# Kernel optimization log

Hardware: AMD Instinct MI355X
Metric: run time of the kernel (lower is better)

The kernel has to match this reference:

```python
import jax, jax.numpy as jnp
import numpy as np

B, L, D = 2, 1024, 1024
N = 64                 # ssm_state_dim
R = (D + 15) // 16     # dt_rank = ceil(dim/16) = 64
EPS = 1e-6


def setup_inputs() -> dict:
    key = jax.random.key(0)
    ks = jax.random.split(key, 12)
    s = 0.02
    return {
        "x": jax.random.normal(ks[0], (B, L, D), dtype=jnp.float32),
        "norm_w": jnp.ones((D,), jnp.float32),
        "Wx": jax.random.normal(ks[1], (R + 2 * N, D), jnp.float32) * s,
        "dtW": jax.random.normal(ks[2], (D, R), jnp.float32) * s,
        "dtb": jax.random.normal(ks[3], (D,), jnp.float32) * s,
        "A_log": jnp.zeros((D, N), jnp.float32),
        "Dskip": jnp.ones((D,), jnp.float32),
        "Wout": jax.random.normal(ks[4], (D, D), jnp.float32) * s,
        "selW": jax.random.normal(ks[5], (D, D), jnp.float32) * s,
        "selb": jax.random.normal(ks[6], (D,), jnp.float32) * s,
        "sel_gate": jnp.ones((D,), jnp.float32),
        "impW": jax.random.normal(ks[7], (N, D), jnp.float32) * s,
        "impb": jax.random.normal(ks[8], (N,), jnp.float32) * s,
        "gateW": jax.random.normal(ks[9], (D, D), jnp.float32) * s,
        "gateb": jax.random.normal(ks[10], (D,), jnp.float32) * s,
    }


def _rmsnorm(x, w):
    return x * jax.lax.rsqrt(jnp.mean(x * x, axis=-1, keepdims=True) + EPS) * w


def reference(x, norm_w, Wx, dtW, dtb, A_log, Dskip, Wout, selW, selb,
              sel_gate, impW, impb, gateW, gateb):
    xn = _rmsnorm(x, norm_w)                       # [B,L,D]
    xp = jnp.einsum('bld,kd->blk', xn, Wx)         # [B,L,R+2N]
    delta_r = xp[..., :R]
    B_ssm = xp[..., R:R + N]
    C_ssm = xp[..., R + N:]

    # selective masking
    sel = jax.nn.sigmoid((jnp.einsum('bld,kd->blk', xn, selW) + selb) * sel_gate)
    xn = xn * sel
    imp = jax.nn.sigmoid(jnp.einsum('bld,nd->bln', xn, impW) + impb)  # [B,L,N]

    delta = jax.nn.softplus(jnp.einsum('blr,dr->bld', delta_r, dtW) + dtb)  # [B,L,D]
    A = -jnp.exp(A_log)                            # [D,N]

    # gated update
    gate = jax.nn.sigmoid(jnp.einsum('bld,kd->blk', xn, gateW) + gateb)
    xn = xn * gate

    B_ssm = B_ssm * imp
    C_ssm = C_ssm * imp

    def step(h, inp):
        dt, bt, ct, xt = inp                       # [B,D],[B,N],[B,N],[B,D]
        dA = jnp.exp(dt[:, :, None] * A)           # [B,D,N]
        h = dA * h + dt[:, :, None] * bt[:, None, :] * xt[:, :, None]
        y = jnp.einsum('bdn,bn->bd', h, ct)
        return h, y

    h0 = jnp.zeros((B, D, N), x.dtype)
    xs = (jnp.moveaxis(delta, 1, 0), jnp.moveaxis(B_ssm, 1, 0),
          jnp.moveaxis(C_ssm, 1, 0), jnp.moveaxis(xn, 1, 0))
    _, ys = jax.lax.scan(step, h0, xs)             # ys: [L,B,D]
    y = jnp.moveaxis(ys, 0, 1)                     # [B,L,D]

    return jnp.einsum('bld,kd->blk', y + x * Dskip, Wout)
```

## Files before the change

kernel.cpp:

```cpp
#include <hip/hip_runtime.h>

typedef __attribute__((ext_vector_type(8))) short short8;
typedef __attribute__((ext_vector_type(4))) float f32x4;
typedef unsigned short u16;

__device__ __forceinline__ u16 f2bf(float f){
  unsigned int u = __float_as_uint(f);
  u += 0x7FFFu + ((u>>16)&1u);
  return (u16)(u>>16);
}
__device__ __forceinline__ float bf2f(u16 h){
  return __uint_as_float(((unsigned int)h)<<16);
}
__device__ __forceinline__ float sigm(float x){ return 1.f/(1.f+__expf(-x)); }

__device__ __forceinline__ float fexp2(float x){
#if __has_builtin(__builtin_amdgcn_exp2f)
  return __builtin_amdgcn_exp2f(x);
#else
  float r; asm("v_exp_f32 %0, %1" : "=v"(r) : "v"(x)); return r;
#endif
}

__device__ __forceinline__ void gl_lds(const u16* g, u16* l){
  __builtin_amdgcn_global_load_lds(
      (const __attribute__((address_space(1))) void*)g,
      (__attribute__((address_space(3))) void*)l, 16, 0, 0);
}

#define MDIM 2048
#define DDIM 1024
#define KDIM 1024
#define LOG2E 1.44269504f
#define NCHUNK 32
#define TCH 32
#define CVT_TOTAL 3473408

__global__ __launch_bounds__(256) void pre_k(
    const float* __restrict__ x, const float* __restrict__ nw,
    const float* __restrict__ selW, const float* __restrict__ Wx,
    const float* __restrict__ gateW, const float* __restrict__ impW,
    const float* __restrict__ Wout, const float* __restrict__ dtW,
    u16* __restrict__ xn,
    u16* __restrict__ dA, u16* __restrict__ dB, u16* __restrict__ dC,
    u16* __restrict__ dD)
{
  const int bx = blockIdx.x, tid = threadIdx.x;
  if (bx < 2048){
    float4 xv = ((const float4*)(x + (size_t)bx*DDIM))[tid];
    float s = xv.x*xv.x + xv.y*xv.y + xv.z*xv.z + xv.w*xv.w;
    #pragma unroll
    for (int m=1; m<64; m<<=1) s += __shfl_xor(s, m);
    __shared__ float red[4];
    if ((tid&63)==0) red[tid>>6] = s;
    __syncthreads();
    float tot = red[0]+red[1]+red[2]+red[3];
    float rs = rsqrtf(tot*(1.f/1024.f) + 1e-6f);
    float4 wv = ((const float4*)nw)[tid];
    ushort4 o;
    o.x=f2bf(xv.x*rs*wv.x); o.y=f2bf(xv.y*rs*wv.y);
    o.z=f2bf(xv.z*rs*wv.z); o.w=f2bf(xv.w*rs*wv.w);
    ((ushort4*)(xn + (size_t)bx*DDIM))[tid] = o;
  } else {
    int e = ((bx-2048)*256 + tid)*4;
    if (e >= CVT_TOTAL) return;
    const float4* s; u16* d;
    if (e < 1048576){ s=(const float4*)(selW+e); d=dA+e; }
    else if (e < 1245184){ int o=e-1048576; s=(const float4*)(Wx+o); d=dA+1048576+o; }
    else if (e < 2293760){ int o=e-1245184; s=(const float4*)(gateW+o); d=dB+o; }
    else if (e < 2359296){ int o=e-2293760; s=(const float4*)(impW+o); d=dB+1048576+o; }
    else if (e < 3407872){ int o=e-2359296; s=(const float4*)(Wout+o); d=dC+o; }
    else { int o=e-3407872; s=(const float4*)(dtW+o); d=dD+o; }
    float4 v = *s;
    ushort4 ov; ov.x=f2bf(v.x); ov.y=f2bf(v.y); ov.z=f2bf(v.z); ov.w=f2bf(v.w);
    *(ushort4*)d = ov;
  }
}

template<int MODE>
__device__ __forceinline__ void gemm_body(
    u16* smem,
    const u16* __restrict__ X, const u16* __restrict__ W,
    const float* __restrict__ b1, const float* __restrict__ b2,
    const float* __restrict__ b3, const u16* __restrict__ aux,
    u16* __restrict__ oBF, u16* __restrict__ oBF2,
    float* __restrict__ oF1, float* __restrict__ oF2, float* __restrict__ oF3)
{
  u16* const AsP[3] = { smem, smem + 4096, smem + 8192 };
  u16* const BsP[3] = { smem + 12288, smem + 16384, smem + 20480 };
  const int tid = threadIdx.x;
  const int wid = tid>>6, lane = tid&63;
  const int wr = wid>>1, wc = wid&1;
  const int lr = lane&15, lg = lane>>4;

  const int nx = gridDim.x;
  const int nwg = nx*gridDim.y;
  const int lin = blockIdx.y*nx + blockIdx.x;
  const int lt = (lin&7)*(nwg>>3) + (lin>>3);
  const int bm = (lt/nx)*64, bn = (lt%nx)*64;

  f32x4 acc[2][2];
  #pragma unroll
  for (int a0=0;a0<2;++a0)
    #pragma unroll
    for (int b0=0;b0<2;++b0) acc[a0][b0] = (f32x4){0.f,0.f,0.f,0.f};

  const int srow = wid*8 + (lane>>3);
  const int kslot = 8*((lane&7) ^ (lane>>3));
  const u16* ag = X + (size_t)(bm + srow)*KDIM + kslot;
  const u16* bg = W + (size_t)(bn + srow)*KDIM + kslot;
  const int lofs = wid*512;

  auto stage = [&](int buf, int kt){
    gl_lds(ag + kt, AsP[buf] + lofs);
    gl_lds(ag + (size_t)32*KDIM + kt, AsP[buf] + 2048 + lofs);
    gl_lds(bg + kt, BsP[buf] + lofs);
    gl_lds(bg + (size_t)32*KDIM + kt, BsP[buf] + 2048 + lofs);
  };

  stage(0, 0);
  stage(1, 64);
  stage(2, 128);
  asm volatile("s_waitcnt vmcnt(8)" ::: "memory");
  __builtin_amdgcn_s_barrier();

  #pragma unroll
  for (int t=0; t<16; ++t){
    const int cur = t % 3;
    short8 af[2][2], bfr[2][2];
    #pragma unroll
    for (int a0=0;a0<2;++a0){
      const int R = wr*32 + a0*16 + lr;
      #pragma unroll
      for (int kh=0;kh<2;++kh)
        af[a0][kh] = *(const short8*)(AsP[cur] + R*64 + ((kh*32 + lg*8) ^ ((lr&7)<<3)));
    }
    #pragma unroll
    for (int b0=0;b0<2;++b0){
      const int R = wc*32 + b0*16 + lr;
      #pragma unroll
      for (int kh=0;kh<2;++kh)
        bfr[b0][kh] = *(const short8*)(BsP[cur] + R*64 + ((kh*32 + lg*8) ^ ((lr&7)<<3)));
    }
    asm volatile("s_waitcnt lgkmcnt(0)" ::: "memory");
    __builtin_amdgcn_sched_barrier(0);
    __builtin_amdgcn_s_barrier();
    if (t < 13)
      stage(cur, (t+3)*64);
    #pragma unroll
    for (int kh=0;kh<2;++kh)
      #pragma unroll
      for (int a0=0;a0<2;++a0)
        #pragma unroll
        for (int b0=0;b0<2;++b0)
          acc[a0][b0] = __builtin_amdgcn_mfma_f32_16x16x32_bf16(af[a0][kh], bfr[b0][kh], acc[a0][b0], 0, 0, 0);
    __builtin_amdgcn_sched_barrier(0);
    if (t < 13){
      asm volatile("s_waitcnt vmcnt(8)" ::: "memory");
      __builtin_amdgcn_s_barrier();
    } else if (t == 13){
      asm volatile("s_waitcnt vmcnt(4)" ::: "memory");
      __builtin_amdgcn_s_barrier();
    } else if (t == 14){
      asm volatile("s_waitcnt vmcnt(0)" ::: "memory");
      __builtin_amdgcn_s_barrier();
    }
  }

  const int colb = bn + wc*32;
  #pragma unroll
  for (int a0=0;a0<2;++a0){
    const int m0 = bm + wr*32 + a0*16 + lg*4;
    #pragma unroll
    for (int b0=0;b0<2;++b0){
      const int n = colb + b0*16 + lr;
      #pragma unroll
      for (int i=0;i<4;++i){
        const int m = m0 + i;
        float v = acc[a0][b0][i];
        if constexpr (MODE==0){
          if (n < 1024){
            float s = sigm((v + b1[n])*b2[n]);
            float xnv = bf2f(aux[(size_t)m*1024 + n]);
            oBF[(size_t)m*1024 + n] = f2bf(xnv*s);
          } else if (n < 1088){
            oBF2[(size_t)m*64 + (n-1024)] = f2bf(v);
          } else {
            oF2[(size_t)m*128 + (n-1088)] = v;
          }
        } else if constexpr (MODE==1){
          if (n < 1024){
            float g = sigm(v + b1[n]);
            oBF[(size_t)m*1024 + n] = f2bf(bf2f(aux[(size_t)m*1024 + n])*g);
          } else {
            int c = n-1024;
            float it = sigm(v + b2[c]);
            float bb = b3[(size_t)m*128 + c];
            float cc = b3[(size_t)m*128 + 64 + c];
            oF2[(size_t)m*64 + c] = bb*it;
            oF3[(size_t)m*64 + c] = cc*it;
          }
        } else {
          oF1[(size_t)m*1024 + n] = v;
        }
      }
    }
  }
}

template<int MODE>
__global__ __launch_bounds__(256) void gemm_bt(
    const u16* __restrict__ X, const u16* __restrict__ W,
    const float* __restrict__ b1, const float* __restrict__ b2,
    const float* __restrict__ b3, const u16* __restrict__ aux,
    u16* __restrict__ oBF, u16* __restrict__ oBF2,
    float* __restrict__ oF1, float* __restrict__ oF2, float* __restrict__ oF3)
{
  __shared__ __align__(16) u16 pool[24576];
  gemm_body<MODE>(pool, X, W, b1, b2, b3, aux, oBF, oBF2, oF1, oF2, oF3);
}

__global__ __launch_bounds__(256) void gemm1d_k(
    const u16* __restrict__ xn2, const u16* __restrict__ wsB,
    const float* __restrict__ gateb, const float* __restrict__ impb,
    const float* __restrict__ BCb,
    u16* __restrict__ xn316, float* __restrict__ BIp, float* __restrict__ CIp,
    const u16* __restrict__ dr, const u16* __restrict__ dtWb,
    const float* __restrict__ dtb, u16* __restrict__ delta16)
{
  __shared__ __align__(16) u16 pool[24576];
  if (blockIdx.z == 0){
    gemm_body<1>(pool, xn2, wsB, gateb, impb, BCb, xn2,
                 xn316, nullptr, nullptr, BIp, CIp);
    return;
  }
  if (blockIdx.x >= 16) return;
  u16* As = pool;
  u16* Bs = pool + 4096;
  const int tid = threadIdx.x;
  const int wid = tid>>6, lane = tid&63;
  const int wr = wid>>1, wc = wid&1;
  const int lr = lane&15, lg = lane>>4;
  const int bm = blockIdx.y*64, bn = blockIdx.x*64;

  const int srow = wid*8 + (lane>>3);
  const int kslot = 8*((lane&7) ^ (lane>>3));
  const u16* ag = dr   + (size_t)(bm + srow)*64 + kslot;
  const u16* bg = dtWb + (size_t)(bn + srow)*64 + kslot;
  const int lofs = wid*512;

  gl_lds(ag, As + lofs);
  gl_lds(ag + 32*64, As + 2048 + lofs);
  gl_lds(bg, Bs + lofs);
  gl_lds(bg + 32*64, Bs + 2048 + lofs);
  asm volatile("s_waitcnt vmcnt(0)" ::: "memory");
  __builtin_amdgcn_s_barrier();

  f32x4 acc[2][2];
  #pragma unroll
  for (int a0=0;a0<2;++a0)
    #pragma unroll
    for (int b0=0;b0<2;++b0) acc[a0][b0] = (f32x4){0.f,0.f,0.f,0.f};

  short8 af[2][2], bfr[2][2];
  #pragma unroll
  for (int a0=0;a0<2;++a0){
    const int R = wr*32 + a0*16 + lr;
    #pragma unroll
    for (int kh=0;kh<2;++kh)
      af[a0][kh] = *(const short8*)(As + R*64 + ((kh*32 + lg*8) ^ ((lr&7)<<3)));
  }
  #pragma unroll
  for (int b0=0;b0<2;++b0){
    const int R = wc*32 + b0*16 + lr;
    #pragma unroll
    for (int kh=0;kh<2;++kh)
      bfr[b0][kh] = *(const short8*)(Bs + R*64 + ((kh*32 + lg*8) ^ ((lr&7)<<3)));
  }
  #pragma unroll
  for (int kh=0;kh<2;++kh)
    #pragma unroll
    for (int a0=0;a0<2;++a0)
      #pragma unroll
      for (int b0=0;b0<2;++b0)
        acc[a0][b0] = __builtin_amdgcn_mfma_f32_16x16x32_bf16(af[a0][kh], bfr[b0][kh], acc[a0][b0], 0, 0, 0);

  #pragma unroll
  for (int a0=0;a0<2;++a0){
    const int m0 = bm + wr*32 + a0*16 + lg*4;
    #pragma unroll
    for (int b0=0;b0<2;++b0){
      const int n = bn + wc*32 + b0*16 + lr;
      const float bias = dtb[n];
      #pragma unroll
      for (int i=0;i<4;++i){
        float t = acc[a0][b0][i] + bias;
        float sp = fmaxf(t,0.f) + log1pf(__expf(-fabsf(t)));
        delta16[(size_t)(m0+i)*1024 + n] = f2bf(sp);
      }
    }
  }
}

__global__ __launch_bounds__(256) void scan_p1(
    const u16* __restrict__ delta, const u16* __restrict__ xn3,
    const float* __restrict__ BI, const float* __restrict__ A_log,
    u16* __restrict__ hst, float* __restrict__ sumdt)
{
  const int tid = threadIdx.x;
  const int lane = tid & 63;
  const int wv = __builtin_amdgcn_readfirstlane(tid >> 6);
  const int dg = blockIdx.x, c = blockIdx.y, b = blockIdx.z;
  const int d = dg*64 + lane;
  const int nb = wv*16;
  float A2[16], h[16];
  #pragma unroll
  for (int n0=0;n0<4;++n0){
    float4 al = *(const float4*)(A_log + (size_t)d*64 + nb + n0*4);
    A2[n0*4+0] = -__expf(al.x)*LOG2E;
    A2[n0*4+1] = -__expf(al.y)*LOG2E;
    A2[n0*4+2] = -__expf(al.z)*LOG2E;
    A2[n0*4+3] = -__expf(al.w)*LOG2E;
  }
  #pragma unroll
  for (int n=0;n<16;++n) h[n]=0.f;
  const int row0 = b*1024 + c*TCH;
  float sdt = 0.f;
  #pragma unroll 2
  for (int t=0;t<TCH;++t){
    const size_t row = row0 + t;
    float dt = bf2f(delta[row*1024 + d]);
    float xt = bf2f(xn3[row*1024 + d]);
    sdt += dt;
    float k = dt*xt;
    const float* bi = BI + row*64 + nb;
    #pragma unroll
    for (int n=0;n<16;++n)
      h[n] = fexp2(dt*A2[n])*h[n] + k*bi[n];
  }
  if (wv==0) sumdt[(size_t)(c*2+b)*1024 + d] = sdt;
  #pragma unroll
  for (int n=0;n<16;++n)
    hst[(size_t)((c*2+b)*64 + nb + n)*1024 + d] = f2bf(h[n]);
}

__global__ __launch_bounds__(256) void scan_p2(
    const float* __restrict__ A_log, const float* __restrict__ sumdt,
    u16* __restrict__ hst)
{
  int gid = blockIdx.x*256 + threadIdx.x;
  int d = gid & 1023, n = (gid>>10)&63, b = gid>>16;
  float A2 = -__expf(A_log[(size_t)d*64 + n])*LOG2E;
  const size_t hbase = (size_t)b*65536 + n*1024 + d;
  const size_t sbase = (size_t)b*1024 + d;
  float P[NCHUNK], he[NCHUNK];
  #pragma unroll
  for (int c=0;c<NCHUNK;++c){
    P[c]  = fexp2(A2 * sumdt[sbase + (size_t)c*2048]);
    he[c] = bf2f(hst[hbase + (size_t)c*131072]);
  }
  float carry = 0.f;
  #pragma unroll
  for (int c=0;c<NCHUNK;++c){
    hst[hbase + (size_t)c*131072] = f2bf(carry);
    carry = fmaf(P[c], carry, he[c]);
  }
}

__global__ __launch_bounds__(256) void scan_p3(
    const u16* __restrict__ delta, const u16* __restrict__ xn3,
    const float* __restrict__ BI, const float* __restrict__ CI,
    const float* __restrict__ A_log, const float* __restrict__ x,
    const float* __restrict__ Dskip, const u16* __restrict__ hst,
    u16* __restrict__ z)
{
  __shared__ float ypart[4][TCH][64];
  const int tid = threadIdx.x;
  const int lane = tid & 63;
  const int wv = __builtin_amdgcn_readfirstlane(tid >> 6);
  const int dg = blockIdx.x, c = blockIdx.y, b = blockIdx.z;
  const int d = dg*64 + lane;
  const int nb = wv*16;
  float A2[16], h[16];
  #pragma unroll
  for (int n0=0;n0<4;++n0){
    float4 al = *(const float4*)(A_log + (size_t)d*64 + nb + n0*4);
    A2[n0*4+0] = -__expf(al.x)*LOG2E;
    A2[n0*4+1] = -__expf(al.y)*LOG2E;
    A2[n0*4+2] = -__expf(al.z)*LOG2E;
    A2[n0*4+3] = -__expf(al.w)*LOG2E;
  }
  #pragma unroll
  for (int n=0;n<16;++n)
    h[n] = bf2f(hst[(size_t)((c*2+b)*64 + nb + n)*1024 + d]);
  const int row0 = b*1024 + c*TCH;
  #pragma unroll 2
  for (int t=0;t<TCH;++t){
    const size_t row = row0 + t;
    float dt = bf2f(delta[row*1024 + d]);
    float xt = bf2f(xn3[row*1024 + d]);
    float k = dt*xt;
    const float* bi = BI + row*64 + nb;
    const float* ci = CI + row*64 + nb;
    float y0=0.f, y1=0.f, y2=0.f, y3=0.f;
    #pragma unroll
    for (int n=0;n<16;n+=4){
      h[n+0] = fexp2(dt*A2[n+0])*h[n+0] + k*bi[n+0];  y0 += h[n+0]*ci[n+0];
      h[n+1] = fexp2(dt*A2[n+1])*h[n+1] + k*bi[n+1];  y1 += h[n+1]*ci[n+1];
      h[n+2] = fexp2(dt*A2[n+2])*h[n+2] + k*bi[n+2];  y2 += h[n+2]*ci[n+2];
      h[n+3] = fexp2(dt*A2[n+3])*h[n+3] + k*bi[n+3];  y3 += h[n+3]*ci[n+3];
    }
    ypart[wv][t][lane] = (y0+y1)+(y2+y3);
  }
  __syncthreads();
  const int dbase = dg*64;
  #pragma unroll
  for (int i=0;i<8;++i){
    int idx = tid + i*256;
    int t = idx>>6, dl = idx&63;
    size_t row = row0 + t;
    float y = ypart[0][t][dl] + ypart[1][t][dl] + ypart[2][t][dl] + ypart[3][t][dl];
    float xr = x[row*1024 + dbase + dl];
    z[row*1024 + dbase + dl] = f2bf(y + xr*Dskip[dbase+dl]);
  }
}

extern "C" void kernel_launch(void* const* d_in, const int* in_sizes, int n_in,
                              void* d_out, int out_size, void* d_ws, size_t ws_size,
                              hipStream_t stream) {
  const float* x       = (const float*)d_in[0];
  const float* norm_w  = (const float*)d_in[1];
  const float* Wx      = (const float*)d_in[2];
  const float* dtW     = (const float*)d_in[3];
  const float* dtb     = (const float*)d_in[4];
  const float* A_log   = (const float*)d_in[5];
  const float* Dskip   = (const float*)d_in[6];
  const float* Wout    = (const float*)d_in[7];
  const float* selW    = (const float*)d_in[8];
  const float* selb    = (const float*)d_in[9];
  const float* sel_gate= (const float*)d_in[10];
  const float* impW    = (const float*)d_in[11];
  const float* impb    = (const float*)d_in[12];
  const float* gateW   = (const float*)d_in[13];
  const float* gateb   = (const float*)d_in[14];
  float* out = (float*)d_out;

  char* w = (char*)d_ws;
  u16*  wsA   = (u16*)(w);
  u16*  wsB   = (u16*)(w + 2490368);
  u16*  wsC   = (u16*)(w + 4718592);
  u16*  wsD   = (u16*)(w + 6815744);
  u16*  xn    = (u16*)(w + 6946816);
  u16*  xn2   = (u16*)(w + 11141120);
  u16*  hst   = (u16*)(w + 6946816);
  u16*  dr    = (u16*)(w + 15335424);
  u16*  delta16=(u16*)(w + 15597568);
  u16*  xn316 = (u16*)(w + 19791872);
  float* BCb  = (float*)(w + 23986176);
  float* sdt  = (float*)(w + 23986176);
  float* BIp  = (float*)(w + 25034752);
  float* CIp  = (float*)(w + 25559040);
  u16*  zb    = (u16*)(w + 26083328);

  pre_k<<<2048+3392, 256, 0, stream>>>(x, norm_w, selW, Wx, gateW, impW, Wout, dtW,
                                       xn, wsA, wsB, wsC, wsD);
  gemm_bt<0><<<dim3(19,32), 256, 0, stream>>>(xn, wsA, selb, sel_gate, nullptr, xn,
                                              xn2, dr, nullptr, BCb, nullptr);
  gemm1d_k<<<dim3(17,32,2), 256, 0, stream>>>(xn2, wsB, gateb, impb, BCb,
                                              xn316, BIp, CIp,
                                              dr, wsD, dtb, delta16);
  scan_p1<<<dim3(16,NCHUNK,2), 256, 0, stream>>>(delta16, xn316, BIp, A_log, hst, sdt);
  scan_p2<<<512, 256, 0, stream>>>(A_log, sdt, hst);
  scan_p3<<<dim3(16,NCHUNK,2), 256, 0, stream>>>(delta16, xn316, BIp, CIp, A_log, x, Dskip, hst, zb);
  gemm_bt<2><<<dim3(16,32), 256, 0, stream>>>(zb, wsC, nullptr, nullptr, nullptr, nullptr,
                                              nullptr, nullptr, out, nullptr, nullptr);
}
```

Before: 112.1 us.

## Fuse three scan phases into one cooperative kernel with grid syncs

Merges the chunked-scan local pass, the cross-chunk carry propagation and the output pass into a single cooperative kernel of 512 blocks. Grid-wide syncs replace two kernel launch boundaries. Each block now processes two chunks sequentially, which halves parallelism per phase compared with the prior 1024-block launches. It relies on all 512 blocks being co-resident, and cooperative launch plus grid sync add their own overhead.

```diff
diff --git a/kernel.cpp b/kernel.cpp
--- a/kernel.cpp
+++ b/kernel.cpp
@@ -1,4 +1,6 @@
 #include <hip/hip_runtime.h>
+#include <hip/hip_cooperative_groups.h>
+namespace cg = cooperative_groups;
 
 typedef __attribute__((ext_vector_type(8))) short short8;
 typedef __attribute__((ext_vector_type(4))) float f32x4;
@@ -302,18 +304,22 @@
   }
 }
 
-__global__ __launch_bounds__(256) void scan_p1(
+__global__ __launch_bounds__(256) void fused_scan(
     const u16* __restrict__ delta, const u16* __restrict__ xn3,
-    const float* __restrict__ BI, const float* __restrict__ A_log,
-    u16* __restrict__ hst, float* __restrict__ sumdt)
+    const float* __restrict__ BI, const float* __restrict__ CI,
+    const float* __restrict__ A_log, const float* __restrict__ x,
+    const float* __restrict__ Dskip,
+    u16* __restrict__ hst, float* __restrict__ sumdt, u16* __restrict__ z)
 {
+  __shared__ float ypart[4][TCH][64];
   const int tid = threadIdx.x;
   const int lane = tid & 63;
   const int wv = __builtin_amdgcn_readfirstlane(tid >> 6);
-  const int dg = blockIdx.x, c = blockIdx.y, b = blockIdx.z;
+  const int bid = blockIdx.x;
+  const int dg = bid & 15, cp = (bid>>4) & 15, b = bid>>8;
   const int d = dg*64 + lane;
   const int nb = wv*16;
-  float A2[16], h[16];
+  float A2[16];
   #pragma unroll
   for (int n0=0;n0<4;++n0){
     float4 al = *(const float4*)(A_log + (size_t)d*64 + nb + n0*4);
@@ -322,106 +328,98 @@
     A2[n0*4+2] = -__expf(al.z)*LOG2E;
     A2[n0*4+3] = -__expf(al.w)*LOG2E;
   }
-  #pragma unroll
-  for (int n=0;n<16;++n) h[n]=0.f;
-  const int row0 = b*1024 + c*TCH;
-  float sdt = 0.f;
-  #pragma unroll 2
-  for (int t=0;t<TCH;++t){
-    const size_t row = row0 + t;
-    float dt = bf2f(delta[row*1024 + d]);
-    float xt = bf2f(xn3[row*1024 + d]);
-    sdt += dt;
-    float k = dt*xt;
-    const float* bi = BI + row*64 + nb;
+
+  for (int cc=0; cc<2; ++cc){
+    const int c = cp*2 + cc;
+    float h[16];
+    #pragma unroll
+    for (int n=0;n<16;++n) h[n]=0.f;
+    const int row0 = b*1024 + c*TCH;
+    float sdt = 0.f;
+    #pragma unroll 2
+    for (int t=0;t<TCH;++t){
+      const size_t row = row0 + t;
+      float dt = bf2f(delta[row*1024 + d]);
+      float xt = bf2f(xn3[row*1024 + d]);
+      sdt += dt;
+      float k = dt*xt;
+      const float* bi = BI + row*64 + nb;
+      #pragma unroll
+      for (int n=0;n<16;++n)
+        h[n] = fexp2(dt*A2[n])*h[n] + k*bi[n];
+    }
+    if (wv==0) sumdt[(size_t)(c*2+b)*1024 + d] = sdt;
     #pragma unroll
     for (int n=0;n<16;++n)
-      h[n] = fexp2(dt*A2[n])*h[n] + k*bi[n];
-  }
-  if (wv==0) sumdt[(size_t)(c*2+b)*1024 + d] = sdt;
-  #pragma unroll
-  for (int n=0;n<16;++n)
-    hst[(size_t)((c*2+b)*64 + nb + n)*1024 + d] = f2bf(h[n]);
-}
-
-__global__ __launch_bounds__(256) void scan_p2(
-    const float* __restrict__ A_log, const float* __restrict__ sumdt,
-    u16* __restrict__ hst)
-{
-  int gid = blockIdx.x*256 + threadIdx.x;
-  int d = gid & 1023, n = (gid>>10)&63, b = gid>>16;
-  float A2 = -__expf(A_log[(size_t)d*64 + n])*LOG2E;
-  const size_t hbase = (size_t)b*65536 + n*1024 + d;
-  const size_t sbase = (size_t)b*1024 + d;
-  float P[NCHUNK], he[NCHUNK];
-  #pragma unroll
-  for (int c=0;c<NCHUNK;++c){
-    P[c]  = fexp2(A2 * sumdt[sbase + (size_t)c*2048]);
-    he[c] = bf2f(hst[hbase + (size_t)c*131072]);
-  }
-  float carry = 0.f;
-  #pragma unroll
-  for (int c=0;c<NCHUNK;++c){
-    hst[hbase + (size_t)c*131072] = f2bf(carry);
-    carry = fmaf(P[c], carry, he[c]);
-  }
-}
-
-__global__ __launch_bounds__(256) void scan_p3(
-    const u16* __restrict__ delta, const u16* __restrict__ xn3,
-    const float* __restrict__ BI, const float* __restrict__ CI,
-    const float* __restrict__ A_log, const float* __restrict__ x,
-    const float* __restrict__ Dskip, const u16* __restrict__ hst,
-    u16* __restrict__ z)
-{
-  __shared__ float ypart[4][TCH][64];
-  const int tid = threadIdx.x;
-  const int lane = tid & 63;
-  const int wv = __builtin_amdgcn_readfirstlane(tid >> 6);
-  const int dg = blockIdx.x, c = blockIdx.y, b = blockIdx.z;
-  const int d = dg*64 + lane;
-  const int nb = wv*16;
-  float A2[16], h[16];
-  #pragma unroll
-  for (int n0=0;n0<4;++n0){
-    float4 al = *(const float4*)(A_log + (size_t)d*64 + nb + n0*4);
-    A2[n0*4+0] = -__expf(al.x)*LOG2E;
-    A2[n0*4+1] = -__expf(al.y)*LOG2E;
-    A2[n0*4+2] = -__expf(al.z)*LOG2E;
-    A2[n0*4+3] = -__expf(al.w)*LOG2E;
-  }
-  #pragma unroll
-  for (int n=0;n<16;++n)
-    h[n] = bf2f(hst[(size_t)((c*2+b)*64 + nb + n)*1024 + d]);
-  const int row0 = b*1024 + c*TCH;
-  #pragma unroll 2
-  for (int t=0;t<TCH;++t){
-    const size_t row = row0 + t;
-    float dt = bf2f(delta[row*1024 + d]);
-    float xt = bf2f(xn3[row*1024 + d]);
-    float k = dt*xt;
-    const float* bi = BI + row*64 + nb;
-    const float* ci = CI + row*64 + nb;
-    float y0=0.f, y1=0.f, y2=0.f, y3=0.f;
-    #pragma unroll
-    for (int n=0;n<16;n+=4){
-      h[n+0] = fexp2(dt*A2[n+0])*h[n+0] + k*bi[n+0];  y0 += h[n+0]*ci[n+0];
-      h[n+1] = fexp2(dt*A2[n+1])*h[n+1] + k*bi[n+1];  y1 += h[n+1]*ci[n+1];
-      h[n+2] = fexp2(dt*A2[n+2])*h[n+2] + k*bi[n+2];  y2 += h[n+2]*ci[n+2];
-      h[n+3] = fexp2(dt*A2[n+3])*h[n+3] + k*bi[n+3];  y3 += h[n+3]*ci[n+3];
-    }
-    ypart[wv][t][lane] = (y0+y1)+(y2+y3);
-  }
-  __syncthreads();
+      hst[(size_t)((c*2+b)*64 + nb + n)*1024 + d] = f2bf(h[n]);
+  }
+
+  cg::this_grid().sync();
+
+  {
+    const int gid = bid*256 + tid;
+    const int dd = gid & 1023, n = (gid>>10)&63, bb = gid>>16;
+    float A2b = -__expf(A_log[(size_t)dd*64 + n])*LOG2E;
+    const size_t hbase = (size_t)bb*65536 + n*1024 + dd;
+    const size_t sbase = (size_t)bb*1024 + dd;
+    float carry = 0.f;
+    #pragma unroll
+    for (int half=0; half<2; ++half){
+      float P[16], he[16];
+      #pragma unroll
+      for (int c=0;c<16;++c){
+        int cc = half*16 + c;
+        P[c]  = fexp2(A2b * sumdt[sbase + (size_t)cc*2048]);
+        he[c] = bf2f(hst[hbase + (size_t)cc*131072]);
+      }
+      #pragma unroll
+      for (int c=0;c<16;++c){
+        int cc = half*16 + c;
+        hst[hbase + (size_t)cc*131072] = f2bf(carry);
+        carry = fmaf(P[c], carry, he[c]);
+      }
+    }
+  }
+
+  cg::this_grid().sync();
+
   const int dbase = dg*64;
-  #pragma unroll
-  for (int i=0;i<8;++i){
-    int idx = tid + i*256;
-    int t = idx>>6, dl = idx&63;
-    size_t row = row0 + t;
-    float y = ypart[0][t][dl] + ypart[1][t][dl] + ypart[2][t][dl] + ypart[3][t][dl];
-    float xr = x[row*1024 + dbase + dl];
-    z[row*1024 + dbase + dl] = f2bf(y + xr*Dskip[dbase+dl]);
+  for (int cc=0; cc<2; ++cc){
+    const int c = cp*2 + cc;
+    float h[16];
+    #pragma unroll
+    for (int n=0;n<16;++n)
+      h[n] = bf2f(hst[(size_t)((c*2+b)*64 + nb + n)*1024 + d]);
+    const int row0 = b*1024 + c*TCH;
+    #pragma unroll 2
+    for (int t=0;t<TCH;++t){
+      const size_t row = row0 + t;
+      float dt = bf2f(delta[row*1024 + d]);
+      float xt = bf2f(xn3[row*1024 + d]);
+      float k = dt*xt;
+      const float* bi = BI + row*64 + nb;
+      const float* ci = CI + row*64 + nb;
+      float y0=0.f, y1=0.f, y2=0.f, y3=0.f;
+      #pragma unroll
+      for (int n=0;n<16;n+=4){
+        h[n+0] = fexp2(dt*A2[n+0])*h[n+0] + k*bi[n+0];  y0 += h[n+0]*ci[n+0];
+        h[n+1] = fexp2(dt*A2[n+1])*h[n+1] + k*bi[n+1];  y1 += h[n+1]*ci[n+1];
+        h[n+2] = fexp2(dt*A2[n+2])*h[n+2] + k*bi[n+2];  y2 += h[n+2]*ci[n+2];
+        h[n+3] = fexp2(dt*A2[n+3])*h[n+3] + k*bi[n+3];  y3 += h[n+3]*ci[n+3];
+      }
+      ypart[wv][t][lane] = (y0+y1)+(y2+y3);
+    }
+    __syncthreads();
+    #pragma unroll
+    for (int i=0;i<8;++i){
+      int idx = tid + i*256;
+      int t = idx>>6, dl = idx&63;
+      size_t row = row0 + t;
+      float y = ypart[0][t][dl] + ypart[1][t][dl] + ypart[2][t][dl] + ypart[3][t][dl];
+      float xr = x[row*1024 + dbase + dl];
+      z[row*1024 + dbase + dl] = f2bf(y + xr*Dskip[dbase+dl]);
+    }
+    __syncthreads();
   }
 }
 
@@ -469,9 +467,13 @@
   gemm1d_k<<<dim3(17,32,2), 256, 0, stream>>>(xn2, wsB, gateb, impb, BCb,
                                               xn316, BIp, CIp,
                                               dr, wsD, dtb, delta16);
-  scan_p1<<<dim3(16,NCHUNK,2), 256, 0, stream>>>(delta16, xn316, BIp, A_log, hst, sdt);
-  scan_p2<<<512, 256, 0, stream>>>(A_log, sdt, hst);
-  scan_p3<<<dim3(16,NCHUNK,2), 256, 0, stream>>>(delta16, xn316, BIp, CIp, A_log, x, Dskip, hst, zb);
+  {
+    void* args[] = { (void*)&delta16, (void*)&xn316, (void*)&BIp, (void*)&CIp,
+                     (void*)&A_log, (void*)&x, (void*)&Dskip,
+                     (void*)&hst, (void*)&sdt, (void*)&zb };
+    hipLaunchCooperativeKernel((void*)fused_scan, dim3(512), dim3(256),
+                               args, 0, stream);
+  }
   gemm_bt<2><<<dim3(16,32), 256, 0, stream>>>(zb, wsC, nullptr, nullptr, nullptr, nullptr,
                                               nullptr, nullptr, out, nullptr, nullptr);
 }
```

Measured after the change: 248.1 us. 121% more time.
